# Performance work log

Measured on AMD Instinct MI355X. Metric: run time of the kernel, lower is better.

The kernel has to match this reference:

```python
import jax, jax.numpy as jnp
import numpy as np

S, D_IN, D_OUT = 4096, 1024, 1024

def setup_inputs() -> dict:
    key = jax.random.key(0)
    kx, kq, kk, kv = jax.random.split(key, 4)
    scale = 0.02
    return {
        "x": jax.random.normal(kx, (S, D_IN), dtype=jnp.float32),
        "W_query": jax.random.normal(kq, (D_IN, D_OUT), dtype=jnp.float32) * scale,
        "W_key": jax.random.normal(kk, (D_IN, D_OUT), dtype=jnp.float32) * scale,
        "W_value": jax.random.normal(kv, (D_IN, D_OUT), dtype=jnp.float32) * scale,
    }

def reference(x, W_query, W_key, W_value):
    # x: [S, d_in]; W_*: [d_in, d_out]
    queries = x @ W_query        # [S, d_out]
    keys = x @ W_key             # [S, d_out]
    values = x @ W_value         # [S, d_out]
    d_k = keys.shape[-1]
    attn_scores = queries @ keys.T            # [S, S]
    attn_weights = jax.nn.softmax(attn_scores / jnp.sqrt(jnp.float32(d_k)), axis=-1)
    context_vec = attn_weights @ values       # [S, d_out]
    return context_vec
```

## Files before the change

kernel.cpp:

```cpp
#include <hip/hip_runtime.h>
#include <hip/hip_bf16.h>

typedef _Float16 f16x8 __attribute__((ext_vector_type(8)));
typedef float f32x4 __attribute__((ext_vector_type(4)));
typedef unsigned short u16;
typedef u16 u16x8 __attribute__((ext_vector_type(8)));

__device__ __forceinline__ u16 f2h_bits(float f) {
    _Float16 h = (_Float16)f;
    return __builtin_bit_cast(u16, h);
}
__device__ __forceinline__ float h2f(u16 b) {
    return (float)__builtin_bit_cast(_Float16, b);
}
__device__ __forceinline__ float ld_as_float(const float* p) { return *p; }
__device__ __forceinline__ float ld_as_float(const u16* p)   { return h2f(*p); }

__device__ __forceinline__ void async_ld16(const void* g, void* l) {
    __builtin_amdgcn_global_load_lds(
        (__attribute__((address_space(1))) void*)(void*)g,
        (__attribute__((address_space(3))) void*)l,
        16, 0, 0);
}

__device__ __forceinline__ void store_val(float* p, float v) { *p = v; }
__device__ __forceinline__ void store_val(u16* p, float v)   { *p = f2h_bits(v); }

template <typename OutT, bool EXPSUM>
__global__ __launch_bounds__(256) void gemm_bt(
    const u16* __restrict__ A, int lda,
    const u16* __restrict__ B, int ldb,
    OutT* __restrict__ C, int ldc,
    int Ksplit, float alpha, size_t c_z_stride,
    int bnW, int bmW, int numPanelX, float* __restrict__ rowsum)
{
    __shared__ __attribute__((aligned(16))) u16 As[128 * 64];
    __shared__ __attribute__((aligned(16))) u16 Bs[128 * 64];

    const int t    = threadIdx.x;
    const int lane = t & 63;
    const int wave = t >> 6;
    const int wm   = wave & 1;
    const int wn   = wave >> 1;
    const int l16  = lane & 15;
    const int quad = lane >> 4;

    const int lin = blockIdx.y * gridDim.x + blockIdx.x;
    const int xcd = lin & 7;
    const int idx = lin >> 3;
    const int px  = xcd % numPanelX;
    const int py  = xcd / numPanelX;
    const int bn  = px * bnW + idx % bnW;
    const int bm  = py * bmW + idx / bnW;

    const int kz = blockIdx.z;
    A += (size_t)kz * Ksplit;
    B += (size_t)kz * Ksplit;
    C += (size_t)kz * c_z_stride;

    const int srow = t >> 3;
    const int scol = ((t & 7) ^ ((t >> 3) & 7)) * 8;

    const u16* Ag = A + (size_t)(bm * 128 + srow) * lda + scol;
    const u16* Bg = B + (size_t)(bn * 128 + srow) * ldb + scol;
    const size_t a32 = (size_t)32 * lda;
    const size_t b32 = (size_t)32 * ldb;

    u16* AsD = &As[t * 8];
    u16* BsD = &Bs[t * 8];

    const int p0 = (quad ^ (l16 & 7)) * 8;
    const int p1 = ((quad + 4) ^ (l16 & 7)) * 8;
    const u16* Afr0 = &As[(wm * 64 + l16) * 64 + p0];
    const u16* Afr1 = &As[(wm * 64 + l16) * 64 + p1];
    const u16* Bfr0 = &Bs[(wn * 64 + l16) * 64 + p0];
    const u16* Bfr1 = &Bs[(wn * 64 + l16) * 64 + p1];

    f32x4 acc[4][4] = {};

    for (int k0 = 0; k0 < Ksplit; k0 += 64) {
#pragma unroll
        for (int r = 0; r < 4; r++) {
            async_ld16(Ag + k0 + (size_t)r * a32, AsD + r * 2048);
            async_ld16(Bg + k0 + (size_t)r * b32, BsD + r * 2048);
        }
        __syncthreads();

        f16x8 af[4], bfv[4];
#pragma unroll
        for (int i = 0; i < 4; i++) af[i]  = *(const f16x8*)(Afr0 + i * 1024);
#pragma unroll
        for (int i = 0; i < 4; i++) bfv[i] = *(const f16x8*)(Bfr0 + i * 1024);
#pragma unroll
        for (int mi = 0; mi < 4; mi++)
#pragma unroll
            for (int ni = 0; ni < 4; ni++)
                acc[mi][ni] = __builtin_amdgcn_mfma_f32_16x16x32_f16(
                    af[mi], bfv[ni], acc[mi][ni], 0, 0, 0);
#pragma unroll
        for (int i = 0; i < 4; i++) af[i]  = *(const f16x8*)(Afr1 + i * 1024);
#pragma unroll
        for (int i = 0; i < 4; i++) bfv[i] = *(const f16x8*)(Bfr1 + i * 1024);
#pragma unroll
        for (int mi = 0; mi < 4; mi++)
#pragma unroll
            for (int ni = 0; ni < 4; ni++)
                acc[mi][ni] = __builtin_amdgcn_mfma_f32_16x16x32_f16(
                    af[mi], bfv[ni], acc[mi][ni], 0, 0, 0);

        __syncthreads();
    }

    const int crow = bm * 128 + wm * 64 + quad * 4;
    const int ccol = bn * 128 + wn * 64 + l16;

    if (EXPSUM) {
        float rs[4][4];
#pragma unroll
        for (int mi = 0; mi < 4; mi++)
#pragma unroll
            for (int r = 0; r < 4; r++) rs[mi][r] = 0.f;
#pragma unroll
        for (int mi = 0; mi < 4; mi++) {
#pragma unroll
            for (int ni = 0; ni < 4; ni++) {
#pragma unroll
                for (int r = 0; r < 4; r++) {
                    float e = __expf(acc[mi][ni][r] * alpha);
                    rs[mi][r] += e;
                    store_val(C + (size_t)(crow + mi * 16 + r) * ldc + (ccol + ni * 16), e);
                }
            }
        }
#pragma unroll
        for (int mi = 0; mi < 4; mi++) {
#pragma unroll
            for (int r = 0; r < 4; r++) {
                float s = rs[mi][r];
#pragma unroll
                for (int o = 1; o < 16; o <<= 1) s += __shfl_xor(s, o);
                if (l16 == 0)
                    atomicAdd(&rowsum[crow + mi * 16 + r], s);
            }
        }
    } else {
#pragma unroll
        for (int mi = 0; mi < 4; mi++)
#pragma unroll
            for (int ni = 0; ni < 4; ni++)
#pragma unroll
                for (int r = 0; r < 4; r++) {
                    float v = acc[mi][ni][r] * alpha;
                    store_val(C + (size_t)(crow + mi * 16 + r) * ldc + (ccol + ni * 16), v);
                }
    }
}

__global__ __launch_bounds__(256) void cast_to_f16(
    const float* __restrict__ in, u16* __restrict__ out, int n)
{
    int i = (blockIdx.x * 256 + threadIdx.x) * 4;
    if (i + 3 < n) {
        float4 v = *(const float4*)(in + i);
        ushort4 o;
        o.x = f2h_bits(v.x);
        o.y = f2h_bits(v.y);
        o.z = f2h_bits(v.z);
        o.w = f2h_bits(v.w);
        *(ushort4*)(out + i) = o;
    }
}

__global__ __launch_bounds__(256) void transpose_w3(
    const float* __restrict__ W0, const float* __restrict__ W1,
    const float* __restrict__ W2, u16* __restrict__ out)
{
    const float* in = (blockIdx.z == 0) ? W0 : (blockIdx.z == 1) ? W1 : W2;
    u16* o = out + (size_t)blockIdx.z * 1024 * 1024;
    __shared__ float tile[32][33];
    const int bx = blockIdx.x * 32;
    const int by = blockIdx.y * 32;
    const int tx = threadIdx.x, ty = threadIdx.y;
#pragma unroll
    for (int j = 0; j < 4; j++)
        tile[ty + j * 8][tx] = in[(size_t)(by + ty + j * 8) * 1024 + bx + tx];
    __syncthreads();
#pragma unroll
    for (int j = 0; j < 4; j++)
        o[(size_t)(bx + ty + j * 8) * 1024 + by + tx] = f2h_bits(tile[tx][ty + j * 8]);
}

__global__ __launch_bounds__(256) void transpose_f16(
    const u16* __restrict__ in, int ld_in,
    u16* __restrict__ out, int ld_out)
{
    __shared__ float tile[32][33];
    const int bx = blockIdx.x * 32;
    const int by = blockIdx.y * 32;
    const int tx = threadIdx.x, ty = threadIdx.y;
#pragma unroll
    for (int j = 0; j < 4; j++)
        tile[ty + j * 8][tx] = ld_as_float(&in[(size_t)(by + ty + j * 8) * ld_in + bx + tx]);
    __syncthreads();
#pragma unroll
    for (int j = 0; j < 4; j++)
        out[(size_t)(bx + ty + j * 8) * ld_out + by + tx] = f2h_bits(tile[tx][ty + j * 8]);
}

__global__ __launch_bounds__(256) void zero_f32(float* __restrict__ p, int n)
{
    int i = (blockIdx.x * 256 + threadIdx.x) * 4;
    if (i + 3 < n) *(float4*)(p + i) = float4{0.f, 0.f, 0.f, 0.f};
}

__global__ __launch_bounds__(256) void add_div_f32(
    const float* __restrict__ a, const float* __restrict__ b,
    const float* __restrict__ l, float* __restrict__ o, int n)
{
    int i = (blockIdx.x * 256 + threadIdx.x) * 4;
    if (i + 3 < n) {
        float inv = 1.0f / l[i >> 10];
        float4 x = *(const float4*)(a + i);
        float4 y = *(const float4*)(b + i);
        float4 z;
        z.x = (x.x + y.x) * inv; z.y = (x.y + y.y) * inv;
        z.z = (x.z + y.z) * inv; z.w = (x.w + y.w) * inv;
        *(float4*)(o + i) = z;
    }
}

extern "C" void kernel_launch(void* const* d_in, const int* in_sizes, int n_in,
                              void* d_out, int out_size, void* d_ws, size_t ws_size,
                              hipStream_t stream)
{
    (void)in_sizes; (void)n_in; (void)out_size; (void)ws_size;
    const float* x  = (const float*)d_in[0];
    const float* Wq = (const float*)d_in[1];
    const float* Wk = (const float*)d_in[2];
    const float* Wv = (const float*)d_in[3];
    float* out = (float*)d_out;
    char* ws = (char*)d_ws;

    u16* xb  = (u16*)(ws);
    u16* Wt  = (u16*)(ws + ((size_t)8  << 20));
    u16* QKV = (u16*)(ws + ((size_t)14 << 20));
    u16* Vt  = (u16*)(ws + ((size_t)38 << 20));
    u16* Sb  = (u16*)(ws + ((size_t)46 << 20));
    float* lr = (float*)ws;
    float* P0 = (float*)(ws + ((size_t)6  << 20));
    float* P1 = (float*)(ws + ((size_t)22 << 20));

    const int S = 4096, D = 1024;
    dim3 tb(32, 8);

    cast_to_f16<<<(S * D) / (4 * 256), 256, 0, stream>>>(x, xb, S * D);

    transpose_w3<<<dim3(32, 32, 3), tb, 0, stream>>>(Wq, Wk, Wv, Wt);

    gemm_bt<u16, false><<<dim3(3072 / 128, S / 128, 1), 256, 0, stream>>>(
        xb, D, Wt, D, QKV, 3072, D, 1.0f, 0, 6, 16, 4, nullptr);

    transpose_f16<<<dim3(D / 32, S / 32), tb, 0, stream>>>(
        QKV + 2048, 3072, Vt, S);

    zero_f32<<<S / (4 * 256), 256, 0, stream>>>(lr, S);

    gemm_bt<u16, true><<<dim3(S / 128, S / 128, 1), 256, 0, stream>>>(
        QKV + 0, 3072, QKV + 1024, 3072, Sb, S, D, 0.03125f, 0, 8, 16, 4, lr);

    gemm_bt<float, false><<<dim3(D / 128, S / 128, 2), 256, 0, stream>>>(
        Sb, S, Vt, S, P0, D, 2048, 1.0f, (size_t)(P1 - P0), 4, 8, 2, nullptr);

    add_div_f32<<<(S * D) / (4 * 256), 256, 0, stream>>>(P0, P1, lr, out, S * D);
}
```

Measured before the change: 238.0 us.

## Register-prefetch GEMM with K=32 tiles, fuse V transpose, split-K 4 in fp16

The GEMM main loop moves from direct global-to-LDS async loads with 64-wide K tiles to register-staged prefetch of the next 32-wide K tile, which overlaps the global loads with the MFMA work. LDS use is halved and launch bounds request 4 blocks per CU. The QKV projection now writes V directly in transposed layout, which removes the separate transpose kernel. The PV GEMM uses a 4-way K split that writes fp16 partials, reduced by a new add_div4 kernel, in place of fp32 partials. The fp16 partials add rounding error, and the extra syncthreads per narrower K step could offset the prefetch gains.

```diff
diff --git a/kernel.cpp b/kernel.cpp
--- a/kernel.cpp
+++ b/kernel.cpp
@@ -5,6 +5,7 @@
 typedef float f32x4 __attribute__((ext_vector_type(4)));
 typedef unsigned short u16;
 typedef u16 u16x8 __attribute__((ext_vector_type(8)));
+typedef u16 u16x4 __attribute__((ext_vector_type(4)));
 
 __device__ __forceinline__ u16 f2h_bits(float f) {
     _Float16 h = (_Float16)f;
@@ -13,29 +14,18 @@
 __device__ __forceinline__ float h2f(u16 b) {
     return (float)__builtin_bit_cast(_Float16, b);
 }
-__device__ __forceinline__ float ld_as_float(const float* p) { return *p; }
-__device__ __forceinline__ float ld_as_float(const u16* p)   { return h2f(*p); }
-
-__device__ __forceinline__ void async_ld16(const void* g, void* l) {
-    __builtin_amdgcn_global_load_lds(
-        (__attribute__((address_space(1))) void*)(void*)g,
-        (__attribute__((address_space(3))) void*)l,
-        16, 0, 0);
-}
-
-__device__ __forceinline__ void store_val(float* p, float v) { *p = v; }
-__device__ __forceinline__ void store_val(u16* p, float v)   { *p = f2h_bits(v); }
-
-template <typename OutT, bool EXPSUM>
-__global__ __launch_bounds__(256) void gemm_bt(
+
+template <int MODE>
+__global__ __launch_bounds__(256, 4) void gemm_bt(
     const u16* __restrict__ A, int lda,
     const u16* __restrict__ B, int ldb,
-    OutT* __restrict__ C, int ldc,
+    u16* __restrict__ C, int ldc,
     int Ksplit, float alpha, size_t c_z_stride,
-    int bnW, int bmW, int numPanelX, float* __restrict__ rowsum)
-{
-    __shared__ __attribute__((aligned(16))) u16 As[128 * 64];
-    __shared__ __attribute__((aligned(16))) u16 Bs[128 * 64];
+    int bnW, int bmW, int numPanelX,
+    float* __restrict__ rowsum, u16* __restrict__ vt)
+{
+    __shared__ __attribute__((aligned(16))) u16 As[128 * 32];
+    __shared__ __attribute__((aligned(16))) u16 Bs[128 * 32];
 
     const int t    = threadIdx.x;
     const int lane = t & 63;
@@ -58,63 +48,60 @@
     B += (size_t)kz * Ksplit;
     C += (size_t)kz * c_z_stride;
 
-    const int srow = t >> 3;
-    const int scol = ((t & 7) ^ ((t >> 3) & 7)) * 8;
+    const int srow = t >> 2;
+    const int scol = ((t & 3) ^ ((t >> 3) & 3)) * 8;
 
     const u16* Ag = A + (size_t)(bm * 128 + srow) * lda + scol;
     const u16* Bg = B + (size_t)(bn * 128 + srow) * ldb + scol;
-    const size_t a32 = (size_t)32 * lda;
-    const size_t b32 = (size_t)32 * ldb;
+    const size_t a64 = (size_t)64 * lda;
+    const size_t b64 = (size_t)64 * ldb;
 
     u16* AsD = &As[t * 8];
     u16* BsD = &Bs[t * 8];
 
-    const int p0 = (quad ^ (l16 & 7)) * 8;
-    const int p1 = ((quad + 4) ^ (l16 & 7)) * 8;
-    const u16* Afr0 = &As[(wm * 64 + l16) * 64 + p0];
-    const u16* Afr1 = &As[(wm * 64 + l16) * 64 + p1];
-    const u16* Bfr0 = &Bs[(wn * 64 + l16) * 64 + p0];
-    const u16* Bfr1 = &Bs[(wn * 64 + l16) * 64 + p1];
+    const int fseg = (quad ^ ((l16 >> 1) & 3)) * 8;
+    const u16* Afr = &As[(wm * 64 + l16) * 32 + fseg];
+    const u16* Bfr = &Bs[(wn * 64 + l16) * 32 + fseg];
 
     f32x4 acc[4][4] = {};
-
-    for (int k0 = 0; k0 < Ksplit; k0 += 64) {
-#pragma unroll
-        for (int r = 0; r < 4; r++) {
-            async_ld16(Ag + k0 + (size_t)r * a32, AsD + r * 2048);
-            async_ld16(Bg + k0 + (size_t)r * b32, BsD + r * 2048);
-        }
+    float4 pa0, pa1, pb0, pb1;
+
+    pa0 = *(const float4*)(Ag);
+    pa1 = *(const float4*)(Ag + a64);
+    pb0 = *(const float4*)(Bg);
+    pb1 = *(const float4*)(Bg + b64);
+
+    for (int k0 = 0; k0 < Ksplit; k0 += 32) {
         __syncthreads();
+        *(float4*)(AsD)        = pa0;
+        *(float4*)(AsD + 2048) = pa1;
+        *(float4*)(BsD)        = pb0;
+        *(float4*)(BsD + 2048) = pb1;
+        __syncthreads();
+
+        const int kn = (k0 + 32 < Ksplit) ? k0 + 32 : 0;
+        pa0 = *(const float4*)(Ag + kn);
+        pa1 = *(const float4*)(Ag + kn + a64);
+        pb0 = *(const float4*)(Bg + kn);
+        pb1 = *(const float4*)(Bg + kn + b64);
 
         f16x8 af[4], bfv[4];
 #pragma unroll
-        for (int i = 0; i < 4; i++) af[i]  = *(const f16x8*)(Afr0 + i * 1024);
-#pragma unroll
-        for (int i = 0; i < 4; i++) bfv[i] = *(const f16x8*)(Bfr0 + i * 1024);
+        for (int i = 0; i < 4; i++) af[i]  = *(const f16x8*)(Afr + i * 512);
+#pragma unroll
+        for (int i = 0; i < 4; i++) bfv[i] = *(const f16x8*)(Bfr + i * 512);
 #pragma unroll
         for (int mi = 0; mi < 4; mi++)
 #pragma unroll
             for (int ni = 0; ni < 4; ni++)
                 acc[mi][ni] = __builtin_amdgcn_mfma_f32_16x16x32_f16(
                     af[mi], bfv[ni], acc[mi][ni], 0, 0, 0);
-#pragma unroll
-        for (int i = 0; i < 4; i++) af[i]  = *(const f16x8*)(Afr1 + i * 1024);
-#pragma unroll
-        for (int i = 0; i < 4; i++) bfv[i] = *(const f16x8*)(Bfr1 + i * 1024);
-#pragma unroll
-        for (int mi = 0; mi < 4; mi++)
-#pragma unroll
-            for (int ni = 0; ni < 4; ni++)
-                acc[mi][ni] = __builtin_amdgcn_mfma_f32_16x16x32_f16(
-                    af[mi], bfv[ni], acc[mi][ni], 0, 0, 0);
-
-        __syncthreads();
     }
 
     const int crow = bm * 128 + wm * 64 + quad * 4;
     const int ccol = bn * 128 + wn * 64 + l16;
 
-    if (EXPSUM) {
+    if (MODE == 1) {
         float rs[4][4];
 #pragma unroll
         for (int mi = 0; mi < 4; mi++)
@@ -128,7 +115,7 @@
                 for (int r = 0; r < 4; r++) {
                     float e = __expf(acc[mi][ni][r] * alpha);
                     rs[mi][r] += e;
-                    store_val(C + (size_t)(crow + mi * 16 + r) * ldc + (ccol + ni * 16), e);
+                    C[(size_t)(crow + mi * 16 + r) * ldc + (ccol + ni * 16)] = f2h_bits(e);
                 }
             }
         }
@@ -143,16 +130,27 @@
                     atomicAdd(&rowsum[crow + mi * 16 + r], s);
             }
         }
+    } else if (MODE == 2 && bn >= 16) {
+#pragma unroll
+        for (int ni = 0; ni < 4; ni++) {
+            const int cV = (bn - 16) * 128 + wn * 64 + ni * 16 + l16;
+#pragma unroll
+            for (int mi = 0; mi < 4; mi++) {
+                u16x4 o;
+#pragma unroll
+                for (int r = 0; r < 4; r++) o[r] = f2h_bits(acc[mi][ni][r]);
+                *(u16x4*)(vt + (size_t)cV * 4096 + crow + mi * 16) = o;
+            }
+        }
     } else {
 #pragma unroll
         for (int mi = 0; mi < 4; mi++)
 #pragma unroll
             for (int ni = 0; ni < 4; ni++)
 #pragma unroll
-                for (int r = 0; r < 4; r++) {
-                    float v = acc[mi][ni][r] * alpha;
-                    store_val(C + (size_t)(crow + mi * 16 + r) * ldc + (ccol + ni * 16), v);
-                }
+                for (int r = 0; r < 4; r++)
+                    C[(size_t)(crow + mi * 16 + r) * ldc + (ccol + ni * 16)] =
+                        f2h_bits(acc[mi][ni][r] * alpha);
     }
 }
 
@@ -190,43 +188,30 @@
         o[(size_t)(bx + ty + j * 8) * 1024 + by + tx] = f2h_bits(tile[tx][ty + j * 8]);
 }
 
-__global__ __launch_bounds__(256) void transpose_f16(
-    const u16* __restrict__ in, int ld_in,
-    u16* __restrict__ out, int ld_out)
-{
-    __shared__ float tile[32][33];
-    const int bx = blockIdx.x * 32;
-    const int by = blockIdx.y * 32;
-    const int tx = threadIdx.x, ty = threadIdx.y;
-#pragma unroll
-    for (int j = 0; j < 4; j++)
-        tile[ty + j * 8][tx] = ld_as_float(&in[(size_t)(by + ty + j * 8) * ld_in + bx + tx]);
-    __syncthreads();
-#pragma unroll
-    for (int j = 0; j < 4; j++)
-        out[(size_t)(bx + ty + j * 8) * ld_out + by + tx] = f2h_bits(tile[tx][ty + j * 8]);
-}
-
 __global__ __launch_bounds__(256) void zero_f32(float* __restrict__ p, int n)
 {
     int i = (blockIdx.x * 256 + threadIdx.x) * 4;
     if (i + 3 < n) *(float4*)(p + i) = float4{0.f, 0.f, 0.f, 0.f};
 }
 
-__global__ __launch_bounds__(256) void add_div_f32(
-    const float* __restrict__ a, const float* __restrict__ b,
-    const float* __restrict__ l, float* __restrict__ o, int n)
-{
-    int i = (blockIdx.x * 256 + threadIdx.x) * 4;
-    if (i + 3 < n) {
-        float inv = 1.0f / l[i >> 10];
-        float4 x = *(const float4*)(a + i);
-        float4 y = *(const float4*)(b + i);
-        float4 z;
-        z.x = (x.x + y.x) * inv; z.y = (x.y + y.y) * inv;
-        z.z = (x.z + y.z) * inv; z.w = (x.w + y.w) * inv;
-        *(float4*)(o + i) = z;
-    }
+__global__ __launch_bounds__(256) void add_div4(
+    const u16* __restrict__ P, const float* __restrict__ l,
+    float* __restrict__ o)
+{
+    const size_t zs = (size_t)4096 * 1024;
+    int i = (blockIdx.x * 256 + threadIdx.x) * 8;
+    float inv = 1.0f / l[i >> 10];
+    float s[8] = {};
+#pragma unroll
+    for (int z = 0; z < 4; z++) {
+        u16x8 h = *(const u16x8*)(P + z * zs + i);
+#pragma unroll
+        for (int j = 0; j < 8; j++) s[j] += h2f(h[j]);
+    }
+    float4 lo{s[0] * inv, s[1] * inv, s[2] * inv, s[3] * inv};
+    float4 hi{s[4] * inv, s[5] * inv, s[6] * inv, s[7] * inv};
+    *(float4*)(o + i) = lo;
+    *(float4*)(o + i + 4) = hi;
 }
 
 extern "C" void kernel_launch(void* const* d_in, const int* in_sizes, int n_in,
@@ -243,12 +228,11 @@
 
     u16* xb  = (u16*)(ws);
     u16* Wt  = (u16*)(ws + ((size_t)8  << 20));
-    u16* QKV = (u16*)(ws + ((size_t)14 << 20));
-    u16* Vt  = (u16*)(ws + ((size_t)38 << 20));
-    u16* Sb  = (u16*)(ws + ((size_t)46 << 20));
-    float* lr = (float*)ws;
-    float* P0 = (float*)(ws + ((size_t)6  << 20));
-    float* P1 = (float*)(ws + ((size_t)22 << 20));
+    u16* QK  = (u16*)(ws + ((size_t)14 << 20));
+    u16* Sb  = (u16*)(ws + ((size_t)32 << 20));
+    u16* Vt  = (u16*)(ws + ((size_t)64 << 20));
+    float* lr = (float*)(ws + ((size_t)72 << 20));
+    u16* P   = (u16*)(ws);
 
     const int S = 4096, D = 1024;
     dim3 tb(32, 8);
@@ -257,19 +241,16 @@
 
     transpose_w3<<<dim3(32, 32, 3), tb, 0, stream>>>(Wq, Wk, Wv, Wt);
 
-    gemm_bt<u16, false><<<dim3(3072 / 128, S / 128, 1), 256, 0, stream>>>(
-        xb, D, Wt, D, QKV, 3072, D, 1.0f, 0, 6, 16, 4, nullptr);
-
-    transpose_f16<<<dim3(D / 32, S / 32), tb, 0, stream>>>(
-        QKV + 2048, 3072, Vt, S);
+    gemm_bt<2><<<dim3(3072 / 128, S / 128, 1), 256, 0, stream>>>(
+        xb, D, Wt, D, QK, 2048, D, 1.0f, 0, 6, 16, 4, nullptr, Vt);
 
     zero_f32<<<S / (4 * 256), 256, 0, stream>>>(lr, S);
 
-    gemm_bt<u16, true><<<dim3(S / 128, S / 128, 1), 256, 0, stream>>>(
-        QKV + 0, 3072, QKV + 1024, 3072, Sb, S, D, 0.03125f, 0, 8, 16, 4, lr);
-
-    gemm_bt<float, false><<<dim3(D / 128, S / 128, 2), 256, 0, stream>>>(
-        Sb, S, Vt, S, P0, D, 2048, 1.0f, (size_t)(P1 - P0), 4, 8, 2, nullptr);
-
-    add_div_f32<<<(S * D) / (4 * 256), 256, 0, stream>>>(P0, P1, lr, out, S * D);
-}
+    gemm_bt<1><<<dim3(S / 128, S / 128, 1), 256, 0, stream>>>(
+        QK, 2048, QK + 1024, 2048, Sb, S, D, 0.03125f, 0, 8, 16, 4, lr, nullptr);
+
+    gemm_bt<0><<<dim3(D / 128, S / 128, 4), 256, 0, stream>>>(
+        Sb, S, Vt, S, P, D, 1024, 1.0f, (size_t)S * D, 4, 8, 2, nullptr, nullptr);
+
+    add_div4<<<(S * D) / (8 * 256), 256, 0, stream>>>(P, lr, out);
+}
```

Measured after the change: 230.2 us. 1.03x faster.
